# Optimization experiments

Measured on AMD Instinct MI355X. Metric: run time of the kernel, lower is better.

## Reference

```python
import jax, jax.numpy as jnp
import numpy as np

N_NODES = 100000
N_EDGES = 3200000

def setup_inputs() -> dict:
    key = jax.random.key(0)
    ks = jax.random.split(key, 13)
    d_in, d1, d2, fm_dims, n_cls = 512, 256, 128, 64, 64
    sc = lambda d: 1.0 / np.sqrt(d)
    return {
        'x': jax.random.normal(ks[0], (N_NODES, d_in), jnp.float32),
        'edge_val': jax.random.uniform(ks[1], (N_EDGES,), jnp.float32),
        'W0': jax.random.normal(ks[2], (d_in, d1), jnp.float32) * sc(d_in),
        'W1': jax.random.normal(ks[3], (d1, d2), jnp.float32) * sc(d1),
        'v0_0': jax.random.normal(ks[4], (d1, 1), jnp.float32) * sc(d1),
        'v0_1': jax.random.normal(ks[5], (d1, 1), jnp.float32) * sc(d1),
        'v1_0': jax.random.normal(ks[6], (d2, 1), jnp.float32) * sc(d2),
        'v1_1': jax.random.normal(ks[7], (d2, 1), jnp.float32) * sc(d2),
        'fm_emb': jax.random.normal(ks[8], (d_in, fm_dims), jnp.float32) * sc(d_in),
        'proj_W': jax.random.normal(ks[9], (d2 + fm_dims, n_cls), jnp.float32) * sc(d2 + fm_dims),
        'proj_b': jnp.zeros((n_cls,), jnp.float32),
        'edge_src': jax.random.randint(ks[10], (N_EDGES,), 0, N_NODES, jnp.int32),
        'edge_dst': jax.random.randint(ks[11], (N_EDGES,), 0, N_NODES, jnp.int32),
    }


def gat_layer(H, W, va, vb, src, dst, a_val, n_nodes):
    # H: [N, d_in] -> Hw: [N, d_out]
    Hw = H @ W
    f1 = (Hw @ va)[:, 0]  # [N]
    f2 = (Hw @ vb)[:, 0]  # [N]
    # per-edge logit: A_ij * f1_i + A_ij * f2_j  (tf sparse broadcast mul + sparse_add)
    logits = a_val * (f1[src] + f2[dst])  # [E]
    s = jax.nn.sigmoid(logits)
    # sparse row softmax over outgoing edges of each src node (stable)
    m = jax.ops.segment_max(s, src, num_segments=n_nodes)  # [N]
    e = jnp.exp(s - m[src])
    denom = jax.ops.segment_sum(e, src, num_segments=n_nodes)  # [N]
    att = e / denom[src]  # [E]
    # aggregate: out[i] = sum_j att_ij * Hw[j]
    out = jax.ops.segment_sum(att[:, None] * Hw[dst], src, num_segments=n_nodes)
    return out


def reference(x, edge_val, W0, W1, v0_0, v0_1, v1_0, v1_1, fm_emb, proj_W, proj_b, edge_src, edge_dst):
    n = x.shape[0]
    # two stacked GAT encoder layers (dropout = 0 at inference)
    H = gat_layer(x, W0, v0_0, v0_1, edge_src, edge_dst, edge_val, n)
    H = gat_layer(H, W1, v1_0, v1_1, edge_src, edge_dst, edge_val, n)
    # NFM bilinear pooling: 0.5 * ((x E)^2 - x (E*E))
    summed = x @ fm_emb
    sq_sum = x @ jnp.square(fm_emb)
    nfm = 0.5 * (jnp.square(summed) - sq_sum)
    # projection to logits
    return jnp.concatenate([H, nfm], axis=1) @ proj_W + proj_b
```

## Files before the change

### kernel.cpp

```cpp
#include <hip/hip_runtime.h>


__device__ __forceinline__ int wave_prefix_incl(int v) {
  int lane = threadIdx.x & 63;
#pragma unroll
  for (int d = 1; d < 64; d <<= 1) {
    int n = __shfl_up(v, d);
    if (lane >= d) v += n;
  }
  return v;
}

__device__ __forceinline__ unsigned short f2bf(float f) {
  unsigned int x = __float_as_uint(f);
  x += 0x7fffu + ((x >> 16) & 1u);
  return (unsigned short)(x >> 16);
}
__device__ __forceinline__ float bf2f(unsigned short u) {
  return __uint_as_float(((unsigned int)u) << 16);
}


__global__ void k_hist(const int* __restrict__ src, int* __restrict__ cnt, int E) {
  int e = blockIdx.x * blockDim.x + threadIdx.x;
  if (e < E) atomicAdd(&cnt[src[e]], 1);
}

__global__ void k_scan1(const int* __restrict__ cnt, int* __restrict__ row_ptr,
                        int* __restrict__ partials, int N) {
  int t = threadIdx.x;
  int base = blockIdx.x * 512 + t * 2;
  int e0 = (base < N) ? cnt[base] : 0;
  int e1 = (base + 1 < N) ? cnt[base + 1] : 0;
  int v = e0 + e1;
  int lane = t & 63, wid = t >> 6;
  int incl = wave_prefix_incl(v);
  __shared__ int wsum[4];
  if (lane == 63) wsum[wid] = incl;
  __syncthreads();
  int off = 0;
#pragma unroll
  for (int i = 0; i < 4; ++i)
    if (i < wid) off += wsum[i];
  incl += off;
  int excl = incl - v;
  if (base < N) row_ptr[base] = excl;
  if (base + 1 < N) row_ptr[base + 1] = excl + e0;
  if (t == 255) partials[blockIdx.x] = incl;
}

__global__ void k_scan2(int* partials, int P) {
  int t = threadIdx.x;
  int v = (t < P) ? partials[t] : 0;
  int lane = t & 63, wid = t >> 6;
  int incl = wave_prefix_incl(v);
  __shared__ int wsum[4];
  if (lane == 63) wsum[wid] = incl;
  __syncthreads();
  int off = 0;
#pragma unroll
  for (int i = 0; i < 4; ++i)
    if (i < wid) off += wsum[i];
  incl += off;
  if (t < P) partials[t] = incl - v;
}

__global__ void k_scan3(int* __restrict__ row_ptr, int* __restrict__ cursor,
                        const int* __restrict__ partials, int N, int E) {
  int i = blockIdx.x * blockDim.x + threadIdx.x;
  if (i < N) {
    int v = row_ptr[i] + partials[i >> 9];
    row_ptr[i] = v;
    cursor[i] = v;
  }
  if (i == 0) row_ptr[N] = E;
}

__global__ void k_scatter(const int* __restrict__ src, int* __restrict__ cursor,
                          int* __restrict__ eid, int E) {
  int e = blockIdx.x * blockDim.x + threadIdx.x;
  if (e < E) {
    int p = atomicAdd(&cursor[src[e]], 1);
    eid[p] = e;
  }
}


template <int BM, int BN, int BK>
__global__ __launch_bounds__(256) void k_gemm(const float* __restrict__ A,
                                              const float* __restrict__ B,
                                              float* __restrict__ C, int M, int N,
                                              int K) {
  __shared__ float As[BK][BM];
  __shared__ float Bs[BK][BN];
  int t = threadIdx.x;
  int bm0 = blockIdx.x * BM, bn0 = blockIdx.y * BN;
  int tr = t >> 4, tc = t & 15;
  int row0 = tr * 8, col0 = tc * 4;
  float acc[8][4] = {};
  for (int k0 = 0; k0 < K; k0 += BK) {
#pragma unroll
    for (int i = 0; i < 2; ++i) {
      int s = t + i * 256;
      int ar = s >> 2, akq = (s & 3) * 4;
      int grow = bm0 + ar;
      if (grow >= M) grow = M - 1;
      const float4 av =
          *reinterpret_cast<const float4*>(&A[(size_t)grow * K + k0 + akq]);
      As[akq + 0][ar] = av.x;
      As[akq + 1][ar] = av.y;
      As[akq + 2][ar] = av.z;
      As[akq + 3][ar] = av.w;
    }
    {
      int br = t >> 4, bc = (t & 15) * 4;
      const float4 bv =
          *reinterpret_cast<const float4*>(&B[(size_t)(k0 + br) * N + bn0 + bc]);
      *reinterpret_cast<float4*>(&Bs[br][bc]) = bv;
    }
    __syncthreads();
#pragma unroll
    for (int k = 0; k < BK; ++k) {
      float a0[8], b0[4];
      *reinterpret_cast<float4*>(&a0[0]) =
          *reinterpret_cast<const float4*>(&As[k][row0]);
      *reinterpret_cast<float4*>(&a0[4]) =
          *reinterpret_cast<const float4*>(&As[k][row0 + 4]);
      *reinterpret_cast<float4*>(&b0[0]) =
          *reinterpret_cast<const float4*>(&Bs[k][col0]);
#pragma unroll
      for (int i = 0; i < 8; ++i)
#pragma unroll
        for (int j = 0; j < 4; ++j) acc[i][j] = fmaf(a0[i], b0[j], acc[i][j]);
    }
    __syncthreads();
  }
#pragma unroll
  for (int i = 0; i < 8; ++i) {
    int grow = bm0 + row0 + i;
    if (grow < M) {
      float4 v = {acc[i][0], acc[i][1], acc[i][2], acc[i][3]};
      *reinterpret_cast<float4*>(&C[(size_t)grow * N + bn0 + col0]) = v;
    }
  }
}

template <int BM, int BN, int BK>
__global__ __launch_bounds__(256) void k_gemm_bias(const float* __restrict__ A,
                                                   const float* __restrict__ B,
                                                   const float* __restrict__ bias,
                                                   float* __restrict__ C, int M,
                                                   int N, int K) {
  __shared__ float As[BK][BM];
  __shared__ float Bs[BK][BN];
  int t = threadIdx.x;
  int bm0 = blockIdx.x * BM, bn0 = blockIdx.y * BN;
  int tr = t >> 4, tc = t & 15;
  int row0 = tr * 8, col0 = tc * 4;
  float acc[8][4] = {};
  for (int k0 = 0; k0 < K; k0 += BK) {
#pragma unroll
    for (int i = 0; i < 2; ++i) {
      int s = t + i * 256;
      int ar = s >> 2, akq = (s & 3) * 4;
      int grow = bm0 + ar;
      if (grow >= M) grow = M - 1;
      const float4 av =
          *reinterpret_cast<const float4*>(&A[(size_t)grow * K + k0 + akq]);
      As[akq + 0][ar] = av.x;
      As[akq + 1][ar] = av.y;
      As[akq + 2][ar] = av.z;
      As[akq + 3][ar] = av.w;
    }
    {
      int br = t >> 4, bc = (t & 15) * 4;
      const float4 bv =
          *reinterpret_cast<const float4*>(&B[(size_t)(k0 + br) * N + bn0 + bc]);
      *reinterpret_cast<float4*>(&Bs[br][bc]) = bv;
    }
    __syncthreads();
#pragma unroll
    for (int k = 0; k < BK; ++k) {
      float a0[8], b0[4];
      *reinterpret_cast<float4*>(&a0[0]) =
          *reinterpret_cast<const float4*>(&As[k][row0]);
      *reinterpret_cast<float4*>(&a0[4]) =
          *reinterpret_cast<const float4*>(&As[k][row0 + 4]);
      *reinterpret_cast<float4*>(&b0[0]) =
          *reinterpret_cast<const float4*>(&Bs[k][col0]);
#pragma unroll
      for (int i = 0; i < 8; ++i)
#pragma unroll
        for (int j = 0; j < 4; ++j) acc[i][j] = fmaf(a0[i], b0[j], acc[i][j]);
    }
    __syncthreads();
  }
  const float4 bv = *reinterpret_cast<const float4*>(&bias[bn0 + col0]);
#pragma unroll
  for (int i = 0; i < 8; ++i) {
    int grow = bm0 + row0 + i;
    if (grow < M) {
      float4 v = {acc[i][0] + bv.x, acc[i][1] + bv.y, acc[i][2] + bv.z,
                  acc[i][3] + bv.w};
      *reinterpret_cast<float4*>(&C[(size_t)grow * N + bn0 + col0]) = v;
    }
  }
}

__global__ __launch_bounds__(256) void k_nfm(const float* __restrict__ X,
                                             const float* __restrict__ Emb,
                                             float* __restrict__ out, int M,
                                             int K, int ldo) {
  const int BM = 128, BN = 64, BK = 16;
  __shared__ float As[BK][BM];
  __shared__ float Bs[BK][BN];
  int t = threadIdx.x;
  int bm0 = blockIdx.x * BM;
  int tr = t >> 4, tc = t & 15;
  int row0 = tr * 8, col0 = tc * 4;
  float accS[8][4] = {}, accQ[8][4] = {};
  for (int k0 = 0; k0 < K; k0 += BK) {
#pragma unroll
    for (int i = 0; i < 2; ++i) {
      int s = t + i * 256;
      int ar = s >> 2, akq = (s & 3) * 4;
      int grow = bm0 + ar;
      if (grow >= M) grow = M - 1;
      const float4 av =
          *reinterpret_cast<const float4*>(&X[(size_t)grow * K + k0 + akq]);
      As[akq + 0][ar] = av.x;
      As[akq + 1][ar] = av.y;
      As[akq + 2][ar] = av.z;
      As[akq + 3][ar] = av.w;
    }
    {
      int br = t >> 4, bc = (t & 15) * 4;
      const float4 bv =
          *reinterpret_cast<const float4*>(&Emb[(size_t)(k0 + br) * BN + bc]);
      *reinterpret_cast<float4*>(&Bs[br][bc]) = bv;
    }
    __syncthreads();
#pragma unroll
    for (int k = 0; k < BK; ++k) {
      float a0[8], b0[4], bq[4];
      *reinterpret_cast<float4*>(&a0[0]) =
          *reinterpret_cast<const float4*>(&As[k][row0]);
      *reinterpret_cast<float4*>(&a0[4]) =
          *reinterpret_cast<const float4*>(&As[k][row0 + 4]);
      *reinterpret_cast<float4*>(&b0[0]) =
          *reinterpret_cast<const float4*>(&Bs[k][col0]);
#pragma unroll
      for (int j = 0; j < 4; ++j) bq[j] = b0[j] * b0[j];
#pragma unroll
      for (int i = 0; i < 8; ++i)
#pragma unroll
        for (int j = 0; j < 4; ++j) {
          accS[i][j] = fmaf(a0[i], b0[j], accS[i][j]);
          accQ[i][j] = fmaf(a0[i], bq[j], accQ[i][j]);
        }
    }
    __syncthreads();
  }
#pragma unroll
  for (int i = 0; i < 8; ++i) {
    int grow = bm0 + row0 + i;
    if (grow < M) {
      float4 v;
      v.x = 0.5f * (accS[i][0] * accS[i][0] - accQ[i][0]);
      v.y = 0.5f * (accS[i][1] * accS[i][1] - accQ[i][1]);
      v.z = 0.5f * (accS[i][2] * accS[i][2] - accQ[i][2]);
      v.w = 0.5f * (accS[i][3] * accS[i][3] - accQ[i][3]);
      *reinterpret_cast<float4*>(&out[(size_t)grow * ldo + col0]) = v;
    }
  }
}

__global__ __launch_bounds__(256) void k_cvt_bf16(const float* __restrict__ in,
                                                  unsigned short* __restrict__ out,
                                                  long total) {
  long base = ((long)blockIdx.x * blockDim.x + threadIdx.x) * 8;
  if (base >= total) return;
  float4 a = *reinterpret_cast<const float4*>(&in[base]);
  float4 b = *reinterpret_cast<const float4*>(&in[base + 4]);
  ushort4 lo = {f2bf(a.x), f2bf(a.y), f2bf(a.z), f2bf(a.w)};
  ushort4 hi = {f2bf(b.x), f2bf(b.y), f2bf(b.z), f2bf(b.w)};
  *reinterpret_cast<ushort4*>(&out[base]) = lo;
  *reinterpret_cast<ushort4*>(&out[base + 4]) = hi;
}


template <int D>
__global__ __launch_bounds__(256) void k_fvec(const float* __restrict__ Hw,
                                              const float* __restrict__ va,
                                              const float* __restrict__ vb,
                                              float* __restrict__ f1,
                                              float* __restrict__ f2, int M) {
  int wid = threadIdx.x >> 6, lane = threadIdx.x & 63;
  int i = blockIdx.x * 4 + wid;
  if (i >= M) return;
  const float* row = Hw + (size_t)i * D;
  float s1, s2;
  if (D == 256) {
    float4 h = *reinterpret_cast<const float4*>(&row[lane * 4]);
    float4 a = *reinterpret_cast<const float4*>(&va[lane * 4]);
    float4 b = *reinterpret_cast<const float4*>(&vb[lane * 4]);
    s1 = h.x * a.x + h.y * a.y + h.z * a.z + h.w * a.w;
    s2 = h.x * b.x + h.y * b.y + h.z * b.z + h.w * b.w;
  } else {
    float2 h = *reinterpret_cast<const float2*>(&row[lane * 2]);
    float2 a = *reinterpret_cast<const float2*>(&va[lane * 2]);
    float2 b = *reinterpret_cast<const float2*>(&vb[lane * 2]);
    s1 = h.x * a.x + h.y * a.y;
    s2 = h.x * b.x + h.y * b.y;
  }
#pragma unroll
  for (int d = 32; d; d >>= 1) {
    s1 += __shfl_down(s1, d);
    s2 += __shfl_down(s2, d);
  }
  if (lane == 0) {
    f1[i] = s1;
    f2[i] = s2;
  }
}

__global__ void k_edge_s(const float* __restrict__ aval, const int* __restrict__ src,
                         const int* __restrict__ dst, const float* __restrict__ f1,
                         const float* __restrict__ f2, float* __restrict__ att,
                         float* __restrict__ m, int E) {
  int e = blockIdx.x * blockDim.x + threadIdx.x;
  if (e >= E) return;
  float x = aval[e] * (f1[src[e]] + f2[dst[e]]);
  float s = 1.0f / (1.0f + __expf(-x));
  att[e] = s;
  atomicMax((int*)&m[src[e]], __float_as_int(s));
}

__global__ void k_edge_exp(const int* __restrict__ src, const float* __restrict__ m,
                           float* __restrict__ att, float* __restrict__ denom,
                           int E) {
  int e = blockIdx.x * blockDim.x + threadIdx.x;
  if (e >= E) return;
  float ev = __expf(att[e] - m[src[e]]);
  att[e] = ev;
  atomicAdd(&denom[src[e]], ev);
}

template <int D>
__global__ __launch_bounds__(256) void k_agg(const unsigned short* __restrict__ Hwb,
                                             const float* __restrict__ att,
                                             const int* __restrict__ row_ptr,
                                             const int* __restrict__ eid,
                                             const int* __restrict__ dst,
                                             const float* __restrict__ denom,
                                             float* __restrict__ out, int M,
                                             int ldo) {
  int wid = threadIdx.x >> 6, lane = threadIdx.x & 63;
  int i = blockIdx.x * 4 + wid;
  if (i >= M) return;
  int p0 = __builtin_amdgcn_readfirstlane(row_ptr[i]);
  int p1 = __builtin_amdgcn_readfirstlane(row_ptr[i + 1]);
  if (D == 256) {
    float4 acc = {0.f, 0.f, 0.f, 0.f};
    for (int p = p0; p < p1; ++p) {
      int e = eid[p];
      float w = att[e];
      int j = dst[e];
      ushort4 hv =
          *reinterpret_cast<const ushort4*>(&Hwb[(size_t)j * 256 + lane * 4]);
      acc.x = fmaf(w, bf2f(hv.x), acc.x);
      acc.y = fmaf(w, bf2f(hv.y), acc.y);
      acc.z = fmaf(w, bf2f(hv.z), acc.z);
      acc.w = fmaf(w, bf2f(hv.w), acc.w);
    }
    float inv = (p1 > p0) ? 1.0f / denom[i] : 0.0f;
    float4 o = {acc.x * inv, acc.y * inv, acc.z * inv, acc.w * inv};
    *reinterpret_cast<float4*>(&out[(size_t)i * ldo + lane * 4]) = o;
  } else {
    float2 acc = {0.f, 0.f};
    for (int p = p0; p < p1; ++p) {
      int e = eid[p];
      float w = att[e];
      int j = dst[e];
      unsigned int hv =
          *reinterpret_cast<const unsigned int*>(&Hwb[(size_t)j * 128 + lane * 2]);
      acc.x = fmaf(w, bf2f((unsigned short)(hv & 0xffffu)), acc.x);
      acc.y = fmaf(w, bf2f((unsigned short)(hv >> 16)), acc.y);
    }
    float inv = (p1 > p0) ? 1.0f / denom[i] : 0.0f;
    float2 o = {acc.x * inv, acc.y * inv};
    *reinterpret_cast<float2*>(&out[(size_t)i * ldo + lane * 2]) = o;
  }
}


extern "C" void kernel_launch(void* const* d_in, const int* in_sizes, int n_in,
                              void* d_out, int out_size, void* d_ws, size_t ws_size,
                              hipStream_t stream) {
  (void)n_in;
  (void)out_size;
  const float* x = (const float*)d_in[0];
  const float* aval = (const float*)d_in[1];
  const float* W0 = (const float*)d_in[2];
  const float* W1 = (const float*)d_in[3];
  const float* v00 = (const float*)d_in[4];
  const float* v01 = (const float*)d_in[5];
  const float* v10 = (const float*)d_in[6];
  const float* v11 = (const float*)d_in[7];
  const float* fme = (const float*)d_in[8];
  const float* pW = (const float*)d_in[9];
  const float* pb = (const float*)d_in[10];
  const int* esrc = (const int*)d_in[11];
  const int* edst = (const int*)d_in[12];
  const int N = in_sizes[0] / 512;
  const int E = in_sizes[1];
  float* out = (float*)d_out;

  char* w = (char*)d_ws;
  size_t off = 0;
  auto alloc = [&](size_t bytes) -> char* {
    char* p = w + off;
    off += (bytes + 255) & ~(size_t)255;
    return p;
  };
  float* bufA = (float*)alloc((size_t)N * 256 * 4);
  unsigned short* bufB = (unsigned short*)alloc((size_t)N * 256 * 2);
  float* bufC = (float*)alloc((size_t)N * 128 * 4);
  float* f1 = (float*)alloc((size_t)N * 4);
  float* f2 = (float*)alloc((size_t)N * 4);
  float* mbuf = (float*)alloc((size_t)N * 4);
  float* dnm = (float*)alloc((size_t)N * 4);
  float* att = (float*)alloc((size_t)E * 4);
  int* cnt = (int*)alloc((size_t)N * 4);
  int* rp = (int*)alloc((size_t)(N + 1) * 4);
  int* cur = (int*)alloc((size_t)N * 4);
  int* eid = (int*)alloc((size_t)E * 4);
  int* part = (int*)alloc(4096);
  if (off > ws_size) return;

  float* Hw0 = bufA;
  unsigned short* Hwb0 = bufB;
  float* H1 = bufA;
  float* Hw1 = bufC;
  unsigned short* Hwb1 = bufB;
  float* Hcat = bufA;

  const int TPB = 256;
  int egrid = (E + TPB - 1) / TPB;
  int ngrid4 = (N + 3) / 4;
  int P = (N + 511) / 512;

  hipMemsetAsync(cnt, 0, (size_t)N * 4, stream);
  k_hist<<<egrid, TPB, 0, stream>>>(esrc, cnt, E);
  k_scan1<<<P, TPB, 0, stream>>>(cnt, rp, part, N);
  k_scan2<<<1, TPB, 0, stream>>>(part, P);
  k_scan3<<<(N + TPB) / TPB, TPB, 0, stream>>>(rp, cur, part, N, E);
  k_scatter<<<egrid, TPB, 0, stream>>>(esrc, cur, eid, E);

  {
    dim3 g((N + 127) / 128, 256 / 64);
    k_gemm<128, 64, 16><<<g, TPB, 0, stream>>>(x, W0, Hw0, N, 256, 512);
  }
  k_fvec<256><<<ngrid4, TPB, 0, stream>>>(Hw0, v00, v01, f1, f2, N);
  {
    long total = (long)N * 256;
    int g = (int)((total / 8 + TPB - 1) / TPB);
    k_cvt_bf16<<<g, TPB, 0, stream>>>(Hw0, Hwb0, total);
  }
  hipMemsetAsync(mbuf, 0, (size_t)N * 4, stream);
  hipMemsetAsync(dnm, 0, (size_t)N * 4, stream);
  k_edge_s<<<egrid, TPB, 0, stream>>>(aval, esrc, edst, f1, f2, att, mbuf, E);
  k_edge_exp<<<egrid, TPB, 0, stream>>>(esrc, mbuf, att, dnm, E);
  k_agg<256><<<ngrid4, TPB, 0, stream>>>(Hwb0, att, rp, eid, edst, dnm, H1, N, 256);

  {
    dim3 g((N + 127) / 128, 128 / 64);
    k_gemm<128, 64, 16><<<g, TPB, 0, stream>>>(H1, W1, Hw1, N, 128, 256);
  }
  k_nfm<<<(N + 127) / 128, TPB, 0, stream>>>(x, fme, Hcat + 128, N, 512, 192);
  k_fvec<128><<<ngrid4, TPB, 0, stream>>>(Hw1, v10, v11, f1, f2, N);
  {
    long total = (long)N * 128;
    int g = (int)((total / 8 + TPB - 1) / TPB);
    k_cvt_bf16<<<g, TPB, 0, stream>>>(Hw1, Hwb1, total);
  }
  hipMemsetAsync(mbuf, 0, (size_t)N * 4, stream);
  hipMemsetAsync(dnm, 0, (size_t)N * 4, stream);
  k_edge_s<<<egrid, TPB, 0, stream>>>(aval, esrc, edst, f1, f2, att, mbuf, E);
  k_edge_exp<<<egrid, TPB, 0, stream>>>(esrc, mbuf, att, dnm, E);
  k_agg<128><<<ngrid4, TPB, 0, stream>>>(Hwb1, att, rp, eid, edst, dnm, Hcat, N, 192);

  {
    dim3 g((N + 127) / 128, 1);
    k_gemm_bias<128, 64, 16><<<g, TPB, 0, stream>>>(Hcat, pW, pb, out, N, 64, 192);
  }
}
```

Baseline: 2.771 ms.

## Drop softmax max pass and process multiple edges per wave in aggregation

Since sigmoid outputs are bounded in (0,1), the per-row max subtraction is removed and the two edge kernels are fused into one that computes exp(sigmoid) and accumulates the denominator directly. This eliminates an atomicMax pass, a memset and a reread of the attention array per layer. The aggregation kernel now splits each wave across 2 or 4 edges with 16-byte bf16 loads per lane, reducing partials via cross-lane shuffles. This trades some extra shuffle work for more memory parallelism in the gather.

```diff
diff --git a/kernel.cpp b/kernel.cpp
--- a/kernel.cpp
+++ b/kernel.cpp
@@ -15,9 +15,6 @@
   unsigned int x = __float_as_uint(f);
   x += 0x7fffu + ((x >> 16) & 1u);
   return (unsigned short)(x >> 16);
-}
-__device__ __forceinline__ float bf2f(unsigned short u) {
-  return __uint_as_float(((unsigned int)u) << 16);
 }
 
 
@@ -324,24 +321,15 @@
   }
 }
 
-__global__ void k_edge_s(const float* __restrict__ aval, const int* __restrict__ src,
-                         const int* __restrict__ dst, const float* __restrict__ f1,
-                         const float* __restrict__ f2, float* __restrict__ att,
-                         float* __restrict__ m, int E) {
+__global__ void k_edge(const float* __restrict__ aval, const int* __restrict__ src,
+                       const int* __restrict__ dst, const float* __restrict__ f1,
+                       const float* __restrict__ f2, float* __restrict__ att,
+                       float* __restrict__ denom, int E) {
   int e = blockIdx.x * blockDim.x + threadIdx.x;
   if (e >= E) return;
   float x = aval[e] * (f1[src[e]] + f2[dst[e]]);
   float s = 1.0f / (1.0f + __expf(-x));
-  att[e] = s;
-  atomicMax((int*)&m[src[e]], __float_as_int(s));
-}
-
-__global__ void k_edge_exp(const int* __restrict__ src, const float* __restrict__ m,
-                           float* __restrict__ att, float* __restrict__ denom,
-                           int E) {
-  int e = blockIdx.x * blockDim.x + threadIdx.x;
-  if (e >= E) return;
-  float ev = __expf(att[e] - m[src[e]]);
+  float ev = __expf(s);
   att[e] = ev;
   atomicAdd(&denom[src[e]], ev);
 }
@@ -360,36 +348,57 @@
   if (i >= M) return;
   int p0 = __builtin_amdgcn_readfirstlane(row_ptr[i]);
   int p1 = __builtin_amdgcn_readfirstlane(row_ptr[i + 1]);
+  float acc[8] = {};
   if (D == 256) {
-    float4 acc = {0.f, 0.f, 0.f, 0.f};
-    for (int p = p0; p < p1; ++p) {
+    int half = lane >> 5, q = lane & 31;
+    for (int p = p0 + half; p < p1; p += 2) {
       int e = eid[p];
       float w = att[e];
       int j = dst[e];
-      ushort4 hv =
-          *reinterpret_cast<const ushort4*>(&Hwb[(size_t)j * 256 + lane * 4]);
-      acc.x = fmaf(w, bf2f(hv.x), acc.x);
-      acc.y = fmaf(w, bf2f(hv.y), acc.y);
-      acc.z = fmaf(w, bf2f(hv.z), acc.z);
-      acc.w = fmaf(w, bf2f(hv.w), acc.w);
-    }
-    float inv = (p1 > p0) ? 1.0f / denom[i] : 0.0f;
-    float4 o = {acc.x * inv, acc.y * inv, acc.z * inv, acc.w * inv};
-    *reinterpret_cast<float4*>(&out[(size_t)i * ldo + lane * 4]) = o;
+      uint4 hv =
+          *reinterpret_cast<const uint4*>(&Hwb[(size_t)j * 256 + q * 8]);
+#pragma unroll
+      for (int c = 0; c < 4; ++c) {
+        unsigned int u = (&hv.x)[c];
+        acc[2 * c + 0] = fmaf(w, __uint_as_float(u << 16), acc[2 * c + 0]);
+        acc[2 * c + 1] = fmaf(w, __uint_as_float(u & 0xffff0000u), acc[2 * c + 1]);
+      }
+    }
+#pragma unroll
+    for (int c = 0; c < 8; ++c) acc[c] += __shfl_xor(acc[c], 32);
+    if (half == 0) {
+      float inv = (p1 > p0) ? 1.0f / denom[i] : 0.0f;
+      float4 lo = {acc[0] * inv, acc[1] * inv, acc[2] * inv, acc[3] * inv};
+      float4 hi = {acc[4] * inv, acc[5] * inv, acc[6] * inv, acc[7] * inv};
+      *reinterpret_cast<float4*>(&out[(size_t)i * ldo + q * 8]) = lo;
+      *reinterpret_cast<float4*>(&out[(size_t)i * ldo + q * 8 + 4]) = hi;
+    }
   } else {
-    float2 acc = {0.f, 0.f};
-    for (int p = p0; p < p1; ++p) {
+    int quarter = lane >> 4, q = lane & 15;
+    for (int p = p0 + quarter; p < p1; p += 4) {
       int e = eid[p];
       float w = att[e];
       int j = dst[e];
-      unsigned int hv =
-          *reinterpret_cast<const unsigned int*>(&Hwb[(size_t)j * 128 + lane * 2]);
-      acc.x = fmaf(w, bf2f((unsigned short)(hv & 0xffffu)), acc.x);
-      acc.y = fmaf(w, bf2f((unsigned short)(hv >> 16)), acc.y);
-    }
-    float inv = (p1 > p0) ? 1.0f / denom[i] : 0.0f;
-    float2 o = {acc.x * inv, acc.y * inv};
-    *reinterpret_cast<float2*>(&out[(size_t)i * ldo + lane * 2]) = o;
+      uint4 hv =
+          *reinterpret_cast<const uint4*>(&Hwb[(size_t)j * 128 + q * 8]);
+#pragma unroll
+      for (int c = 0; c < 4; ++c) {
+        unsigned int u = (&hv.x)[c];
+        acc[2 * c + 0] = fmaf(w, __uint_as_float(u << 16), acc[2 * c + 0]);
+        acc[2 * c + 1] = fmaf(w, __uint_as_float(u & 0xffff0000u), acc[2 * c + 1]);
+      }
+    }
+#pragma unroll
+    for (int c = 0; c < 8; ++c) acc[c] += __shfl_xor(acc[c], 32);
+#pragma unroll
+    for (int c = 0; c < 8; ++c) acc[c] += __shfl_xor(acc[c], 16);
+    if (quarter == 0) {
+      float inv = (p1 > p0) ? 1.0f / denom[i] : 0.0f;
+      float4 lo = {acc[0] * inv, acc[1] * inv, acc[2] * inv, acc[3] * inv};
+      float4 hi = {acc[4] * inv, acc[5] * inv, acc[6] * inv, acc[7] * inv};
+      *reinterpret_cast<float4*>(&out[(size_t)i * ldo + q * 8]) = lo;
+      *reinterpret_cast<float4*>(&out[(size_t)i * ldo + q * 8 + 4]) = hi;
+    }
   }
 }
 
@@ -428,7 +437,6 @@
   float* bufC = (float*)alloc((size_t)N * 128 * 4);
   float* f1 = (float*)alloc((size_t)N * 4);
   float* f2 = (float*)alloc((size_t)N * 4);
-  float* mbuf = (float*)alloc((size_t)N * 4);
   float* dnm = (float*)alloc((size_t)N * 4);
   float* att = (float*)alloc((size_t)E * 4);
   int* cnt = (int*)alloc((size_t)N * 4);
@@ -467,10 +475,8 @@
     int g = (int)((total / 8 + TPB - 1) / TPB);
     k_cvt_bf16<<<g, TPB, 0, stream>>>(Hw0, Hwb0, total);
   }
-  hipMemsetAsync(mbuf, 0, (size_t)N * 4, stream);
   hipMemsetAsync(dnm, 0, (size_t)N * 4, stream);
-  k_edge_s<<<egrid, TPB, 0, stream>>>(aval, esrc, edst, f1, f2, att, mbuf, E);
-  k_edge_exp<<<egrid, TPB, 0, stream>>>(esrc, mbuf, att, dnm, E);
+  k_edge<<<egrid, TPB, 0, stream>>>(aval, esrc, edst, f1, f2, att, dnm, E);
   k_agg<256><<<ngrid4, TPB, 0, stream>>>(Hwb0, att, rp, eid, edst, dnm, H1, N, 256);
 
   {
@@ -484,10 +490,8 @@
     int g = (int)((total / 8 + TPB - 1) / TPB);
     k_cvt_bf16<<<g, TPB, 0, stream>>>(Hw1, Hwb1, total);
   }
-  hipMemsetAsync(mbuf, 0, (size_t)N * 4, stream);
   hipMemsetAsync(dnm, 0, (size_t)N * 4, stream);
-  k_edge_s<<<egrid, TPB, 0, stream>>>(aval, esrc, edst, f1, f2, att, mbuf, E);
-  k_edge_exp<<<egrid, TPB, 0, stream>>>(esrc, mbuf, att, dnm, E);
+  k_edge<<<egrid, TPB, 0, stream>>>(aval, esrc, edst, f1, f2, att, dnm, E);
   k_agg<128><<<ngrid4, TPB, 0, stream>>>(Hwb1, att, rp, eid, edst, dnm, Hcat, N, 192);
 
   {
```

Measured after the change: 2.328 ms. 16.0% less time.
